# Optimization experiments

Measured on AMD Instinct MI355X. Metric: run time of the kernel, lower is better.

The kernel has to match this reference:

```python
import jax, jax.numpy as jnp
import numpy as np
from jax import lax

WIN = 9
PAD = WIN // 2
WIN3 = WIN ** 3


def _box_sum(x):
    """Separable 3D box-filter local sum. x: [N, 1, D, H, W].
    Mathematically identical to conv3d with a ones([1,1,WIN,WIN,WIN]) kernel,
    padding=PAD, but done as three 1D passes (O(3*WIN) instead of O(WIN^3))."""
    dn = ('NCDHW', 'OIDHW', 'NCDHW')
    for axis in range(3):  # D, H, W
        kshape = [1, 1, 1, 1, 1]
        kshape[2 + axis] = WIN
        kern = jnp.ones(kshape, dtype=x.dtype)
        padding = [(0, 0), (0, 0), (0, 0)]
        padding[axis] = (PAD, PAD)
        x = lax.conv_general_dilated(x, kern, window_strides=(1, 1, 1),
                                     padding=padding, dimension_numbers=dn)
    return x


def setup_inputs() -> dict:
    key = jax.random.key(0)
    k1, k2 = jax.random.split(key)
    shape = (2, 1, 160, 192, 160)
    predicted = jax.random.normal(k1, shape, dtype=jnp.float32)
    target = jax.random.normal(k2, shape, dtype=jnp.float32)
    return {"predicted": predicted, "target": target}


def reference(predicted, target):
    I = predicted
    J = target
    # Batch the 5 independent box-sums in one conv call by folding into batch.
    stacked = jnp.concatenate([I, J, I * I, J * J, I * J], axis=0)  # [5B,1,D,H,W]
    sums = _box_sum(stacked)
    I_sum, J_sum, I2_sum, J2_sum, IJ_sum = jnp.split(sums, 5, axis=0)

    u_I = I_sum / WIN3
    u_J = J_sum / WIN3

    cross = IJ_sum - u_J * I_sum - u_I * J_sum + u_I * u_J * WIN3
    I_var = I2_sum - 2.0 * u_I * I_sum + u_I * u_I * WIN3
    J_var = J2_sum - 2.0 * u_J * J_sum + u_J * u_J * WIN3

    cc = cross * cross / (I_var * J_var + 1e-05)
    return jnp.mean(cc)
```

## Files before the change

kernel.cpp:

```cpp
#include <hip/hip_runtime.h>

#define Bv   2
#define Dd   160
#define Hh   192
#define Ww   160
#define HW   (Hh*Ww)
#define DHW  (Dd*Hh*Ww)
#define NTOT (Bv*DHW)
#define INV729 (1.0f/729.0f)

typedef _Float16 f16;

__device__ __forceinline__ float4 LD4(const float* p) {
    return *reinterpret_cast<const float4*>(p);
}
__device__ __forceinline__ float4 LD4(const f16* p) {
    union { uint2 u; f16 h[4]; } c;
    c.u = *reinterpret_cast<const uint2*>(p);
    return make_float4((float)c.h[0], (float)c.h[1], (float)c.h[2], (float)c.h[3]);
}
__device__ __forceinline__ void ST4(float* p, float4 v) {
    *reinterpret_cast<float4*>(p) = v;
}
__device__ __forceinline__ void ST4(f16* p, float4 v) {
    union { uint2 u; f16 h[4]; } c;
    c.h[0] = (f16)v.x; c.h[1] = (f16)v.y; c.h[2] = (f16)v.z; c.h[3] = (f16)v.w;
    *reinterpret_cast<uint2*>(p) = c.u;
}
__device__ __forceinline__ float4 add4(float4 a, float4 b) {
    return make_float4(a.x+b.x, a.y+b.y, a.z+b.z, a.w+b.w);
}
__device__ __forceinline__ float4 sub4(float4 a, float4 b) {
    return make_float4(a.x-b.x, a.y-b.y, a.z-b.z, a.w-b.w);
}
__device__ __forceinline__ float4 zero4() { return make_float4(0.f,0.f,0.f,0.f); }

__device__ __forceinline__ void rowsum5(const float* __restrict__ rI,
                                        const float* __restrict__ rJ,
                                        int x0, float sgn, float4 S[5]) {
    float wI[12], wJ[12];
    if (x0 >= 4 && x0 <= Ww - 8) {
        float4 a0 = LD4(rI + x0 - 4), a1 = LD4(rI + x0), a2 = LD4(rI + x0 + 4);
        wI[0]=a0.x; wI[1]=a0.y; wI[2]=a0.z;  wI[3]=a0.w;
        wI[4]=a1.x; wI[5]=a1.y; wI[6]=a1.z;  wI[7]=a1.w;
        wI[8]=a2.x; wI[9]=a2.y; wI[10]=a2.z; wI[11]=a2.w;
        float4 b0 = LD4(rJ + x0 - 4), b1 = LD4(rJ + x0), b2 = LD4(rJ + x0 + 4);
        wJ[0]=b0.x; wJ[1]=b0.y; wJ[2]=b0.z;  wJ[3]=b0.w;
        wJ[4]=b1.x; wJ[5]=b1.y; wJ[6]=b1.z;  wJ[7]=b1.w;
        wJ[8]=b2.x; wJ[9]=b2.y; wJ[10]=b2.z; wJ[11]=b2.w;
    } else {
        #pragma unroll
        for (int i = 0; i < 12; ++i) {
            int xx = x0 - 4 + i;
            bool ok = (xx >= 0) && (xx < Ww);
            wI[i] = ok ? rI[xx] : 0.f;
            wJ[i] = ok ? rJ[xx] : 0.f;
        }
    }
#define CH(cidx, EXPR) {                                                    \
        float t[12];                                                        \
        _Pragma("unroll")                                                   \
        for (int i = 0; i < 12; ++i) {                                      \
            float a = wI[i], b = wJ[i]; (void)a; (void)b;                   \
            t[i] = (EXPR);                                                  \
        }                                                                   \
        float s0 = ((t[0]+t[1])+(t[2]+t[3]))+((t[4]+t[5])+(t[6]+t[7]))+t[8];\
        float s1 = s0 - t[0] + t[9];                                        \
        float s2 = s1 - t[1] + t[10];                                       \
        float s3 = s2 - t[2] + t[11];                                       \
        S[cidx].x += sgn * s0; S[cidx].y += sgn * s1;                       \
        S[cidx].z += sgn * s2; S[cidx].w += sgn * s3;                       \
    }
    CH(0, a); CH(1, b); CH(2, a * a); CH(3, b * b); CH(4, a * b);
#undef CH
}

__device__ __forceinline__ float cc4(const float4 S[5]) {
    float acc = 0.f;
#define FIN(CMP) {                                                      \
        float SI = S[0].CMP, SJ = S[1].CMP, SII = S[2].CMP,             \
              SJJ = S[3].CMP, SIJ = S[4].CMP;                           \
        float uI = SI * INV729, uJ = SJ * INV729;                       \
        float cross = SIJ - uJ * SI - uI * SJ + uI * uJ * 729.0f;       \
        float Iv = SII - 2.0f * uI * SI + uI * uI * 729.0f;             \
        float Jv = SJJ - 2.0f * uJ * SJ + uJ * uJ * 729.0f;             \
        acc += cross * cross / (Iv * Jv + 1e-5f);                       \
    }
    FIN(x) FIN(y) FIN(z) FIN(w)
#undef FIN
    return acc;
}

__device__ __forceinline__ void block_reduce_atomic(float acc, float* out) {
    for (int off = 32; off > 0; off >>= 1) acc += __shfl_down(acc, off);
    __shared__ float red[4];
    int lane = threadIdx.x & 63, wid = threadIdx.x >> 6;
    if (lane == 0) red[wid] = acc;
    __syncthreads();
    if (threadIdx.x == 0)
        atomicAdd(out, (red[0]+red[1]+red[2]+red[3]) * (1.0f/(float)NTOT));
}

template<typename TS>
__global__ __launch_bounds__(256)
void k12_xy(const float* __restrict__ I, const float* __restrict__ J,
            TS* __restrict__ B) {
    int tid = blockIdx.x * 256 + threadIdx.x;
    int x4 = tid % (Ww/4);  int t1 = tid / (Ww/4);
    int yc = t1 % (Hh/8);   t1 /= (Hh/8);
    int z  = t1 % Dd;       int b = t1 / Dd;
    int x0 = x4 * 4, y0 = yc * 8;

    const float* sI = I + (size_t)b * DHW + (size_t)z * HW;
    const float* sJ = J + (size_t)b * DHW + (size_t)z * HW;
    TS* dst = B + (size_t)b * DHW + (size_t)z * HW + x0;

    float4 S[5] = {zero4(), zero4(), zero4(), zero4(), zero4()};
    #pragma unroll
    for (int dy = -4; dy <= 3; ++dy) {
        int y = y0 + dy;
        if (y >= 0) rowsum5(sI + (size_t)y * Ww, sJ + (size_t)y * Ww, x0, 1.f, S);
    }
    #pragma unroll
    for (int y = y0; y < y0 + 8; ++y) {
        int yt = y + 4;
        if (yt < Hh) rowsum5(sI + (size_t)yt * Ww, sJ + (size_t)yt * Ww, x0, 1.f, S);
        ST4(dst + (size_t)y * Ww,                    S[0]);
        ST4(dst + (size_t)NTOT     + (size_t)y * Ww, S[1]);
        ST4(dst + (size_t)2 * NTOT + (size_t)y * Ww, S[2]);
        ST4(dst + (size_t)3 * NTOT + (size_t)y * Ww, S[3]);
        ST4(dst + (size_t)4 * NTOT + (size_t)y * Ww, S[4]);
        int yo = y - 4;
        if (yo >= 0) rowsum5(sI + (size_t)yo * Ww, sJ + (size_t)yo * Ww, x0, -1.f, S);
    }
}

template<typename TS>
__global__ __launch_bounds__(256)
void k3_zpass(const TS* __restrict__ Bb, float* __restrict__ out) {
    int tid = blockIdx.x * 256 + threadIdx.x;
    int x4 = tid % (Ww/4);  int t1 = tid / (Ww/4);
    int y  = t1 % Hh;       t1 /= Hh;
    int zc = t1 % (Dd/8);   int b = t1 / (Dd/8);
    int z0 = zc * 8;

    size_t base = (size_t)b * DHW + (size_t)y * Ww + x4 * 4;
    const TS* P0 = Bb + base;

    float4 S[5] = {zero4(), zero4(), zero4(), zero4(), zero4()};

#define LOADADD(zi) {                                                   \
        const TS* pp = P0 + (size_t)(zi) * HW;                          \
        S[0] = add4(S[0], LD4(pp));                                     \
        S[1] = add4(S[1], LD4(pp + (size_t)NTOT));                      \
        S[2] = add4(S[2], LD4(pp + (size_t)2 * NTOT));                  \
        S[3] = add4(S[3], LD4(pp + (size_t)3 * NTOT));                  \
        S[4] = add4(S[4], LD4(pp + (size_t)4 * NTOT));                  \
    }
#define LOADSUB(zi) {                                                   \
        const TS* pp = P0 + (size_t)(zi) * HW;                          \
        S[0] = sub4(S[0], LD4(pp));                                     \
        S[1] = sub4(S[1], LD4(pp + (size_t)NTOT));                      \
        S[2] = sub4(S[2], LD4(pp + (size_t)2 * NTOT));                  \
        S[3] = sub4(S[3], LD4(pp + (size_t)3 * NTOT));                  \
        S[4] = sub4(S[4], LD4(pp + (size_t)4 * NTOT));                  \
    }

    #pragma unroll
    for (int dz = -4; dz <= 3; ++dz) {
        int z = z0 + dz;
        if (z >= 0) LOADADD(z);
    }

    float acc = 0.f;
    #pragma unroll
    for (int z = z0; z < z0 + 8; ++z) {
        int zt = z + 4;
        if (zt < Dd) LOADADD(zt);
        acc += cc4(S);
        int zo = z - 4;
        if (zo >= 0) LOADSUB(zo);
    }
#undef LOADADD
#undef LOADSUB

    block_reduce_atomic(acc, out);
}

__global__ __launch_bounds__(256)
void k_brute(const float* __restrict__ I, const float* __restrict__ J,
             float* __restrict__ out) {
    int tid = blockIdx.x * 256 + threadIdx.x;
    int x4 = tid % (Ww/4);  int t1 = tid / (Ww/4);
    int y  = t1 % Hh;       t1 /= Hh;
    int z  = t1 % Dd;       int b = t1 / Dd;
    int x0 = x4 * 4;

    const float* bI = I + (size_t)b * DHW;
    const float* bJ = J + (size_t)b * DHW;

    float4 S[5] = {zero4(), zero4(), zero4(), zero4(), zero4()};
    for (int dz = -4; dz <= 4; ++dz) {
        int zz = z + dz;
        if (zz < 0 || zz >= Dd) continue;
        for (int dy = -4; dy <= 4; ++dy) {
            int yy = y + dy;
            if (yy < 0 || yy >= Hh) continue;
            rowsum5(bI + (size_t)zz * HW + (size_t)yy * Ww,
                    bJ + (size_t)zz * HW + (size_t)yy * Ww, x0, 1.f, S);
        }
    }
    block_reduce_atomic(cc4(S), out);
}

extern "C" void kernel_launch(void* const* d_in, const int* in_sizes, int n_in,
                              void* d_out, int out_size, void* d_ws, size_t ws_size,
                              hipStream_t stream) {
    const float* I = (const float*)d_in[0];
    const float* J = (const float*)d_in[1];
    float* out = (float*)d_out;

    hipMemsetAsync(d_out, 0, sizeof(float), stream);

    const int gk = 307200/256;

    if (ws_size >= (size_t)5 * NTOT * sizeof(f16)) {
        f16* B = (f16*)d_ws;
        k12_xy<f16><<<gk, 256, 0, stream>>>(I, J, B);
        k3_zpass<f16><<<gk, 256, 0, stream>>>(B, out);
    } else {
        k_brute<<<(NTOT/4)/256, 256, 0, stream>>>(I, J, out);
    }
}
```

Measured before the change: 235.3 us.

## Replace sliding-window y/z passes with 4-output register windows per thread

Each thread now produces 4 output rows (y pass) or 4 slices (z pass) by loading 12 inputs and adding each into every window it covers, replacing the old 8-output running add/subtract window. Thread count doubles, which adds parallelism and removes the long serial dependency chain. The cost is more redundant input reads (12 loads per 4 outputs instead of 16 per 8) and more registers for the 4x5 float4 accumulators, which may lower occupancy.

```diff
diff --git a/kernel.cpp b/kernel.cpp
--- a/kernel.cpp
+++ b/kernel.cpp
@@ -30,14 +30,11 @@
 __device__ __forceinline__ float4 add4(float4 a, float4 b) {
     return make_float4(a.x+b.x, a.y+b.y, a.z+b.z, a.w+b.w);
 }
-__device__ __forceinline__ float4 sub4(float4 a, float4 b) {
-    return make_float4(a.x-b.x, a.y-b.y, a.z-b.z, a.w-b.w);
-}
 __device__ __forceinline__ float4 zero4() { return make_float4(0.f,0.f,0.f,0.f); }
 
-__device__ __forceinline__ void rowsum5(const float* __restrict__ rI,
-                                        const float* __restrict__ rJ,
-                                        int x0, float sgn, float4 S[5]) {
+__device__ __forceinline__ void xsum5(const float* __restrict__ rI,
+                                      const float* __restrict__ rJ,
+                                      int x0, float4 s[5]) {
     float wI[12], wJ[12];
     if (x0 >= 4 && x0 <= Ww - 8) {
         float4 a0 = LD4(rI + x0 - 4), a1 = LD4(rI + x0), a2 = LD4(rI + x0 + 4);
@@ -68,8 +65,7 @@
         float s1 = s0 - t[0] + t[9];                                        \
         float s2 = s1 - t[1] + t[10];                                       \
         float s3 = s2 - t[2] + t[11];                                       \
-        S[cidx].x += sgn * s0; S[cidx].y += sgn * s1;                       \
-        S[cidx].z += sgn * s2; S[cidx].w += sgn * s3;                       \
+        s[cidx] = make_float4(s0, s1, s2, s3);                              \
     }
     CH(0, a); CH(1, b); CH(2, a * a); CH(3, b * b); CH(4, a * b);
 #undef CH
@@ -103,87 +99,101 @@
 
 template<typename TS>
 __global__ __launch_bounds__(256)
-void k12_xy(const float* __restrict__ I, const float* __restrict__ J,
-            TS* __restrict__ B) {
+void k12v2(const float* __restrict__ I, const float* __restrict__ J,
+           TS* __restrict__ B) {
     int tid = blockIdx.x * 256 + threadIdx.x;
     int x4 = tid % (Ww/4);  int t1 = tid / (Ww/4);
-    int yc = t1 % (Hh/8);   t1 /= (Hh/8);
+    int yg = t1 % (Hh/4);   t1 /= (Hh/4);
     int z  = t1 % Dd;       int b = t1 / Dd;
-    int x0 = x4 * 4, y0 = yc * 8;
+    int x0 = x4 * 4, y0 = yg * 4;
 
     const float* sI = I + (size_t)b * DHW + (size_t)z * HW;
     const float* sJ = J + (size_t)b * DHW + (size_t)z * HW;
     TS* dst = B + (size_t)b * DHW + (size_t)z * HW + x0;
 
-    float4 S[5] = {zero4(), zero4(), zero4(), zero4(), zero4()};
+    float4 W[4][5];
     #pragma unroll
-    for (int dy = -4; dy <= 3; ++dy) {
-        int y = y0 + dy;
-        if (y >= 0) rowsum5(sI + (size_t)y * Ww, sJ + (size_t)y * Ww, x0, 1.f, S);
-    }
+    for (int k = 0; k < 4; ++k)
+        #pragma unroll
+        for (int c = 0; c < 5; ++c) W[k][c] = zero4();
+
+#define ROW(rr) {                                                       \
+        float4 s[5];                                                    \
+        xsum5(sI + (size_t)(y0 - 4 + (rr)) * Ww,                        \
+              sJ + (size_t)(y0 - 4 + (rr)) * Ww, x0, s);                \
+        _Pragma("unroll")                                               \
+        for (int k = 0; k < 4; ++k)                                     \
+            if ((rr) - 8 <= k && k <= (rr)) {                           \
+                _Pragma("unroll")                                       \
+                for (int c = 0; c < 5; ++c)                             \
+                    W[k][c] = add4(W[k][c], s[c]);                      \
+            }                                                           \
+    }
+
+    if (y0 >= 4 && y0 + 7 < Hh) {
+        #pragma unroll
+        for (int rr = 0; rr < 12; ++rr) ROW(rr);
+    } else {
+        #pragma unroll
+        for (int rr = 0; rr < 12; ++rr) {
+            int y = y0 - 4 + rr;
+            if (y >= 0 && y < Hh) ROW(rr);
+        }
+    }
+#undef ROW
+
     #pragma unroll
-    for (int y = y0; y < y0 + 8; ++y) {
-        int yt = y + 4;
-        if (yt < Hh) rowsum5(sI + (size_t)yt * Ww, sJ + (size_t)yt * Ww, x0, 1.f, S);
-        ST4(dst + (size_t)y * Ww,                    S[0]);
-        ST4(dst + (size_t)NTOT     + (size_t)y * Ww, S[1]);
-        ST4(dst + (size_t)2 * NTOT + (size_t)y * Ww, S[2]);
-        ST4(dst + (size_t)3 * NTOT + (size_t)y * Ww, S[3]);
-        ST4(dst + (size_t)4 * NTOT + (size_t)y * Ww, S[4]);
-        int yo = y - 4;
-        if (yo >= 0) rowsum5(sI + (size_t)yo * Ww, sJ + (size_t)yo * Ww, x0, -1.f, S);
+    for (int k = 0; k < 4; ++k) {
+        #pragma unroll
+        for (int c = 0; c < 5; ++c)
+            ST4(dst + (size_t)c * NTOT + (size_t)(y0 + k) * Ww, W[k][c]);
     }
 }
 
 template<typename TS>
 __global__ __launch_bounds__(256)
-void k3_zpass(const TS* __restrict__ Bb, float* __restrict__ out) {
+void k3v2(const TS* __restrict__ Bb, float* __restrict__ out) {
     int tid = blockIdx.x * 256 + threadIdx.x;
     int x4 = tid % (Ww/4);  int t1 = tid / (Ww/4);
     int y  = t1 % Hh;       t1 /= Hh;
-    int zc = t1 % (Dd/8);   int b = t1 / (Dd/8);
-    int z0 = zc * 8;
-
-    size_t base = (size_t)b * DHW + (size_t)y * Ww + x4 * 4;
-    const TS* P0 = Bb + base;
-
-    float4 S[5] = {zero4(), zero4(), zero4(), zero4(), zero4()};
-
-#define LOADADD(zi) {                                                   \
-        const TS* pp = P0 + (size_t)(zi) * HW;                          \
-        S[0] = add4(S[0], LD4(pp));                                     \
-        S[1] = add4(S[1], LD4(pp + (size_t)NTOT));                      \
-        S[2] = add4(S[2], LD4(pp + (size_t)2 * NTOT));                  \
-        S[3] = add4(S[3], LD4(pp + (size_t)3 * NTOT));                  \
-        S[4] = add4(S[4], LD4(pp + (size_t)4 * NTOT));                  \
-    }
-#define LOADSUB(zi) {                                                   \
-        const TS* pp = P0 + (size_t)(zi) * HW;                          \
-        S[0] = sub4(S[0], LD4(pp));                                     \
-        S[1] = sub4(S[1], LD4(pp + (size_t)NTOT));                      \
-        S[2] = sub4(S[2], LD4(pp + (size_t)2 * NTOT));                  \
-        S[3] = sub4(S[3], LD4(pp + (size_t)3 * NTOT));                  \
-        S[4] = sub4(S[4], LD4(pp + (size_t)4 * NTOT));                  \
-    }
-
+    int zg = t1 % (Dd/4);   int b = t1 / (Dd/4);
+    int z0 = zg * 4;
+
+    const TS* P0 = Bb + (size_t)b * DHW + (size_t)y * Ww + x4 * 4;
+
+    float4 W[4][5];
     #pragma unroll
-    for (int dz = -4; dz <= 3; ++dz) {
-        int z = z0 + dz;
-        if (z >= 0) LOADADD(z);
-    }
-
-    float acc = 0.f;
-    #pragma unroll
-    for (int z = z0; z < z0 + 8; ++z) {
-        int zt = z + 4;
-        if (zt < Dd) LOADADD(zt);
-        acc += cc4(S);
-        int zo = z - 4;
-        if (zo >= 0) LOADSUB(zo);
-    }
-#undef LOADADD
-#undef LOADSUB
-
+    for (int k = 0; k < 4; ++k)
+        #pragma unroll
+        for (int c = 0; c < 5; ++c) W[k][c] = zero4();
+
+#define SLICE(ss) {                                                     \
+        const TS* pp = P0 + (size_t)(z0 - 4 + (ss)) * HW;               \
+        float4 v[5];                                                    \
+        _Pragma("unroll")                                               \
+        for (int c = 0; c < 5; ++c) v[c] = LD4(pp + (size_t)c * NTOT);  \
+        _Pragma("unroll")                                               \
+        for (int k = 0; k < 4; ++k)                                     \
+            if ((ss) - 8 <= k && k <= (ss)) {                           \
+                _Pragma("unroll")                                       \
+                for (int c = 0; c < 5; ++c)                             \
+                    W[k][c] = add4(W[k][c], v[c]);                      \
+            }                                                           \
+    }
+
+    if (z0 >= 4 && z0 + 7 < Dd) {
+        #pragma unroll
+        for (int ss = 0; ss < 12; ++ss) SLICE(ss);
+    } else {
+        #pragma unroll
+        for (int ss = 0; ss < 12; ++ss) {
+            int z = z0 - 4 + ss;
+            if (z >= 0 && z < Dd) SLICE(ss);
+        }
+    }
+#undef SLICE
+
+    float acc = cc4(W[0]) + cc4(W[1]) + cc4(W[2]) + cc4(W[3]);
     block_reduce_atomic(acc, out);
 }
 
@@ -206,8 +216,11 @@
         for (int dy = -4; dy <= 4; ++dy) {
             int yy = y + dy;
             if (yy < 0 || yy >= Hh) continue;
-            rowsum5(bI + (size_t)zz * HW + (size_t)yy * Ww,
-                    bJ + (size_t)zz * HW + (size_t)yy * Ww, x0, 1.f, S);
+            float4 s[5];
+            xsum5(bI + (size_t)zz * HW + (size_t)yy * Ww,
+                  bJ + (size_t)zz * HW + (size_t)yy * Ww, x0, s);
+            #pragma unroll
+            for (int c = 0; c < 5; ++c) S[c] = add4(S[c], s[c]);
         }
     }
     block_reduce_atomic(cc4(S), out);
@@ -222,12 +235,12 @@
 
     hipMemsetAsync(d_out, 0, sizeof(float), stream);
 
-    const int gk = 307200/256;
+    const int gk = 614400/256;
 
     if (ws_size >= (size_t)5 * NTOT * sizeof(f16)) {
         f16* B = (f16*)d_ws;
-        k12_xy<f16><<<gk, 256, 0, stream>>>(I, J, B);
-        k3_zpass<f16><<<gk, 256, 0, stream>>>(B, out);
+        k12v2<f16><<<gk, 256, 0, stream>>>(I, J, B);
+        k3v2<f16><<<gk, 256, 0, stream>>>(B, out);
     } else {
         k_brute<<<(NTOT/4)/256, 256, 0, stream>>>(I, J, out);
     }
```

Result: slower. 326.3 us (+38.7%).
